# Performance work log

Hardware: AMD Instinct MI355X
Metric: run time of the kernel (lower is better)

Reference implementation:

```python
import jax, jax.numpy as jnp
import numpy as np

IN_FEATURE = 256
OUT_FEATURE = 128
ALPHA = 0.5  # LeakyReLU negative slope
NEG_BIG = -9e15


def setup_inputs() -> dict:
    key = jax.random.key(0)
    k1, k2, k3, k4 = jax.random.split(key, 4)
    N = 8192
    x = jax.random.normal(k1, (N, IN_FEATURE), dtype=jnp.float32)
    adj = jax.random.randint(k2, (N, N), 0, 2, dtype=jnp.int32)
    stdv = 1.0 / np.sqrt(OUT_FEATURE)
    W = jax.random.uniform(k3, (IN_FEATURE, OUT_FEATURE), dtype=jnp.float32,
                           minval=-stdv, maxval=stdv)
    a = jax.random.uniform(k4, (2 * OUT_FEATURE, 1), dtype=jnp.float32,
                           minval=-stdv, maxval=stdv)
    return {"input": x, "adj": adj, "W": W, "a": a}


def reference(input, adj, W, a):
    # h: [N, F_out]
    h = input @ W
    # Additive attention: cat([h_i, h_j]) @ a == h_i @ a1 + h_j @ a2
    a1 = a[:OUT_FEATURE, 0]   # [F_out]
    a2 = a[OUT_FEATURE:, 0]   # [F_out]
    f1 = h @ a1               # [N]  (row / source contribution)
    f2 = h @ a2               # [N]  (col / target contribution)
    e = jax.nn.leaky_relu(f1[:, None] + f2[None, :], negative_slope=ALPHA)  # [N, N]
    scores = jnp.where(adj > 0, e, NEG_BIG)
    attention = jax.nn.softmax(scores, axis=1)  # [N, N]
    h_prime = attention @ h                     # [N, F_out]
    return jax.nn.elu(h_prime)
```

## Files before the change

kernel.cpp:

```cpp
#include <hip/hip_runtime.h>

#define N_NODES 8192
#define IN_F 256
#define OUT_F 128
#define ALPHA 0.5f
#define JC 8
#define KCHUNK 1024
#define RK 128
#define ROUNDS 8
#define RSTEPS 4

using short8 = __attribute__((ext_vector_type(8))) short;
using f32x4  = __attribute__((ext_vector_type(4))) float;

__device__ __forceinline__ unsigned int f2bf(float f){
  unsigned int u = __float_as_uint(f);
  u += 0x7fffu + ((u >> 16) & 1u);
  return u >> 16;
}
__device__ __forceinline__ float bf2f(short s){
  return __uint_as_float(((unsigned int)(unsigned short)s) << 16);
}

__global__ __launch_bounds__(256) void k_h(const float* __restrict__ x,
                                           const float* __restrict__ W,
                                           float* __restrict__ h){
  __shared__ float xs[16*IN_F];
  const int tid = threadIdx.x;
  const int r0 = blockIdx.x * 16;
  const float4* xg = (const float4*)(x + (size_t)r0*IN_F);
  float4* xl = (float4*)xs;
  #pragma unroll
  for(int i=0;i<4;i++) xl[tid + i*256] = xg[tid + i*256];
  __syncthreads();
  const int wave = tid >> 6, lane = tid & 63;
  float2 acc[4];
  #pragma unroll
  for(int j=0;j<4;j++){ acc[j].x = 0.f; acc[j].y = 0.f; }
  const float2* Wp = (const float2*)W;
  for(int k4=0;k4<IN_F;k4+=4){
    float4 xq[4];
    #pragma unroll
    for(int j=0;j<4;j++) xq[j] = *(const float4*)&xs[(wave*4+j)*IN_F + k4];
    #pragma unroll
    for(int kk=0;kk<4;kk++){
      float2 wv = Wp[(size_t)(k4+kk)*64 + lane];
      #pragma unroll
      for(int j=0;j<4;j++){
        float xv = kk==0?xq[j].x : kk==1?xq[j].y : kk==2?xq[j].z : xq[j].w;
        acc[j].x += xv*wv.x; acc[j].y += xv*wv.y;
      }
    }
  }
  #pragma unroll
  for(int j=0;j<4;j++)
    *(float2*)(h + (size_t)(r0 + wave*4 + j)*OUT_F + lane*2) = acc[j];
}

__global__ __launch_bounds__(256) void k_f(const float* __restrict__ h,
                                           const float* __restrict__ a,
                                           float* __restrict__ f1,
                                           float* __restrict__ f2){
  const int wave = threadIdx.x >> 6, lane = threadIdx.x & 63;
  const int row = blockIdx.x*4 + wave;
  float2 hv = ((const float2*)(h + (size_t)row*OUT_F))[lane];
  float2 a1 = ((const float2*)a)[lane];
  float2 a2 = ((const float2*)(a + OUT_F))[lane];
  float s1 = hv.x*a1.x + hv.y*a1.y;
  float s2 = hv.x*a2.x + hv.y*a2.y;
  #pragma unroll
  for(int off=32; off; off>>=1){
    s1 += __shfl_down(s1, off);
    s2 += __shfl_down(s2, off);
  }
  if(lane == 0){ f1[row] = s1; f2[row] = s2; }
}

#define LDW 132
__global__ __launch_bounds__(256) void k_pack(const float* __restrict__ h,
                                              unsigned short* __restrict__ P){
  __shared__ float ld[32*LDW];
  const int tid = threadIdx.x;
  const int kb = blockIdx.x, j0 = kb*32;
  #pragma unroll
  for(int i=0;i<4;i++){
    int idx = tid + i*256;
    int row = idx >> 5, c4 = (idx & 31)*4;
    *(float4*)&ld[row*LDW + c4] = *(const float4*)(h + (size_t)(j0+row)*OUT_F + c4);
  }
  __syncthreads();
  #pragma unroll
  for(int i=0;i<2;i++){
    int o = tid*2 + i;
    int c = o >> 6, lane = o & 63;
    int q = lane >> 4, n = lane & 15;
    short8 v;
    #pragma unroll
    for(int t=0;t<8;t++) v[t] = (short)f2bf(ld[(q*8+t)*LDW + c*16 + n]);
    *(short8*)(P + ((size_t)(kb*8 + c)*64 + lane)*8) = v;
  }
}

__global__ __launch_bounds__(256, 2) void k_attn(const int* __restrict__ adj,
    const unsigned short* __restrict__ P,
    const float* __restrict__ f1, const float* __restrict__ f2,
    float* __restrict__ part, float* __restrict__ denp){
  __shared__ __align__(16) unsigned short Alds[128*RK];
  __shared__ __align__(16) short Blds[RK*OUT_F];
  __shared__ float f1s[128];
  const int tid = threadIdx.x;
  const int wave = tid >> 6, lane = tid & 63;
  const int m = lane & 15, q = lane >> 4;
  const int jc = blockIdx.x;
  const int r0b = blockIdx.y * 128;
  const int jb = jc * KCHUNK;
  const int kb0 = jc * (KCHUNK/32);
  const int srow = tid >> 5;
  const int sc0  = (tid & 31) * 4;
  const int swz  = ((((sc0 >> 3) ^ srow) << 4) | ((sc0 & 4) << 1));

  if(tid < 128) f1s[tid] = f1[r0b + tid];

  f32x4 acc0[8], acc1[8];
  #pragma unroll
  for(int c=0;c<8;c++){ acc0[c] = (f32x4){0,0,0,0}; acc1[c] = (f32x4){0,0,0,0}; }
  float den0 = 0.f, den1 = 0.f;

  const char* Ab = (const char*)Alds;
  char* Aw = (char*)Alds + swz;
  const int mw = m & 7;
  const int rg0 = wave*32 + m;

  __syncthreads();

  for(int rd=0; rd<ROUNDS; rd++){
    const int kbase = jb + rd*RK;
    const int4* Pb = (const int4*)(P + ((size_t)(kb0 + rd*4) << 12));
    int4* Bl4 = (int4*)Blds;
    #pragma unroll
    for(int i=0;i<8;i++) Bl4[i*256 + tid] = Pb[i*256 + tid];
    float4 fv = *(const float4*)(f2 + kbase + sc0);
    const char* ap = (const char*)adj + (((size_t)(r0b + srow)*N_NODES + kbase + sc0) << 2);
    #pragma unroll 4
    for(int i=0;i<16;i++){
      int4 av = *(const int4*)(ap + ((size_t)i*8*N_NODES << 2));
      float f1v = f1s[i*8 + srow];
      float t0 = f1v + fv.x, t1 = f1v + fv.y, t2 = f1v + fv.z, t3 = f1v + fv.w;
      t0 = t0 > 0.f ? t0 : ALPHA*t0;  t1 = t1 > 0.f ? t1 : ALPHA*t1;
      t2 = t2 > 0.f ? t2 : ALPHA*t2;  t3 = t3 > 0.f ? t3 : ALPHA*t3;
      float w0 = av.x > 0 ? __expf(t0) : 0.f;
      float w1 = av.y > 0 ? __expf(t1) : 0.f;
      float w2 = av.z > 0 ? __expf(t2) : 0.f;
      float w3 = av.w > 0 ? __expf(t3) : 0.f;
      uint2 pk;
      pk.x = f2bf(w0) | (f2bf(w1) << 16);
      pk.y = f2bf(w2) | (f2bf(w3) << 16);
      *(uint2*)(Aw + (i*8 + srow)*(RK*2)) = pk;
    }
    __syncthreads();
    #pragma unroll
    for(int s=0;s<RSTEPS;s++){
      const int gq = ((s*4 + q) ^ mw) << 4;
      short8 A0 = *(const short8*)(Ab + rg0*(RK*2) + gq);
      short8 A1 = *(const short8*)(Ab + (rg0+16)*(RK*2) + gq);
      #pragma unroll
      for(int t=0;t<8;t++){ den0 += bf2f(A0[t]); den1 += bf2f(A1[t]); }
      const short8* Bl = (const short8*)Blds + s*512 + lane;
      #pragma unroll
      for(int c=0;c<8;c++){
        short8 Bf = Bl[c*64];
        acc0[c] = __builtin_amdgcn_mfma_f32_16x16x32_bf16(A0, Bf, acc0[c], 0,0,0);
        acc1[c] = __builtin_amdgcn_mfma_f32_16x16x32_bf16(A1, Bf, acc1[c], 0,0,0);
      }
    }
    __syncthreads();
  }

  den0 += __shfl_down(den0, 32); den0 += __shfl_down(den0, 16);
  den1 += __shfl_down(den1, 32); den1 += __shfl_down(den1, 16);
  const int r0w = r0b + wave*32;
  if(lane < 16){
    denp[(size_t)jc*N_NODES + r0w + lane]      = den0;
    denp[(size_t)jc*N_NODES + r0w + 16 + lane] = den1;
  }
  float* pp = part + (size_t)jc*N_NODES*OUT_F;
  #pragma unroll
  for(int c=0;c<8;c++){
    #pragma unroll
    for(int reg=0;reg<4;reg++){
      pp[(size_t)(r0w + q*4 + reg)*OUT_F      + c*16 + m] = acc0[c][reg];
      pp[(size_t)(r0w + 16 + q*4 + reg)*OUT_F + c*16 + m] = acc1[c][reg];
    }
  }
}

__global__ __launch_bounds__(256) void k_out(const float* __restrict__ part,
    const float* __restrict__ denp, float* __restrict__ out){
  const int idx = blockIdx.x*256 + threadIdx.x;
  const int r = idx >> 7;
  float v = 0.f, d = 0.f;
  #pragma unroll
  for(int p=0;p<JC;p++){
    v += part[(size_t)p*N_NODES*OUT_F + idx];
    d += denp[(size_t)p*N_NODES + r];
  }
  v /= d;
  out[idx] = v > 0.f ? v : (__expf(v) - 1.f);
}

extern "C" void kernel_launch(void* const* d_in, const int* in_sizes, int n_in,
                              void* d_out, int out_size, void* d_ws, size_t ws_size,
                              hipStream_t stream){
  const float* x   = (const float*)d_in[0];
  const int*   adj = (const int*)d_in[1];
  const float* W   = (const float*)d_in[2];
  const float* a   = (const float*)d_in[3];
  char* ws = (char*)d_ws;
  float* h            = (float*)ws;
  unsigned short* P   = (unsigned short*)(ws + (4u<<20));
  float* f1           = (float*)(ws + (6u<<20));
  float* f2           = (float*)(ws + (6u<<20) + (32u<<10));
  float* part         = (float*)(ws + (8u<<20));
  float* denp         = (float*)(ws + (40u<<20));
  float* out          = (float*)d_out;

  k_h<<<512, 256, 0, stream>>>(x, W, h);
  k_f<<<2048, 256, 0, stream>>>(h, a, f1, f2);
  k_pack<<<256, 256, 0, stream>>>(h, P);
  k_attn<<<dim3(JC,64), 256, 0, stream>>>(adj, P, f1, f2, part, denp);
  k_out<<<(N_NODES*OUT_F)/256, 256, 0, stream>>>(part, denp, out);
}
```

Before: 410.3 us.

## Double-buffer adj and P via async global-to-LDS loads, compute weights in registers

The attention kernel now uses global_load_lds to stream adjacency tiles and packed h tiles straight into double-buffered shared memory, prefetching the next round while the current one is processed. The round size drops from 128 to 32 columns. Each lane reads its adj values in MFMA fragment order from a swizzled LDS layout and computes the bf16 attention weights in registers, which removes the LDS write and reread of the A tile. The denominator is now summed from fp32 weights instead of rounded bf16 values. In exchange the kernel uses more shared memory and takes more barriers, and it depends on the load-to-LDS completion being waited on before each barrier.

```diff
diff --git a/kernel.cpp b/kernel.cpp
--- a/kernel.cpp
+++ b/kernel.cpp
@@ -6,9 +6,8 @@
 #define ALPHA 0.5f
 #define JC 8
 #define KCHUNK 1024
-#define RK 128
-#define ROUNDS 8
-#define RSTEPS 4
+#define RK 32
+#define ROUNDS 32
 
 using short8 = __attribute__((ext_vector_type(8))) short;
 using f32x4  = __attribute__((ext_vector_type(4))) float;
@@ -18,8 +17,11 @@
   u += 0x7fffu + ((u >> 16) & 1u);
   return u >> 16;
 }
-__device__ __forceinline__ float bf2f(short s){
-  return __uint_as_float(((unsigned int)(unsigned short)s) << 16);
+
+__device__ __forceinline__ void gld16(const void* g, void* l){
+  __builtin_amdgcn_global_load_lds(
+      (const __attribute__((address_space(1))) unsigned int*)g,
+      (__attribute__((address_space(3))) unsigned int*)l, 16, 0, 0);
 }
 
 __global__ __launch_bounds__(256) void k_h(const float* __restrict__ x,
@@ -105,8 +107,9 @@
     const unsigned short* __restrict__ P,
     const float* __restrict__ f1, const float* __restrict__ f2,
     float* __restrict__ part, float* __restrict__ denp){
-  __shared__ __align__(16) unsigned short Alds[128*RK];
-  __shared__ __align__(16) short Blds[RK*OUT_F];
+  __shared__ __align__(16) char Alds[2][16384];
+  __shared__ __align__(16) char Blds[2][8192];
+  __shared__ float f2s[KCHUNK];
   __shared__ float f1s[128];
   const int tid = threadIdx.x;
   const int wave = tid >> 6, lane = tid & 63;
@@ -114,64 +117,76 @@
   const int jc = blockIdx.x;
   const int r0b = blockIdx.y * 128;
   const int jb = jc * KCHUNK;
-  const int kb0 = jc * (KCHUNK/32);
-  const int srow = tid >> 5;
-  const int sc0  = (tid & 31) * 4;
-  const int swz  = ((((sc0 >> 3) ^ srow) << 4) | ((sc0 & 4) << 1));
-
+
+  ((float4*)f2s)[tid] = ((const float4*)(f2 + jb))[tid];
   if(tid < 128) f1s[tid] = f1[r0b + tid];
+
+  const int g = (lane & 7) ^ (lane >> 3);
+  const char* asrc[4];
+  #pragma unroll
+  for(int i=0;i<4;i++){
+    int rowid = (wave*4 + i)*8 + (lane >> 3);
+    asrc[i] = (const char*)(adj + (size_t)(r0b + rowid)*N_NODES + jb) + g*16;
+  }
+  const char* bsrc[2];
+  #pragma unroll
+  for(int i=0;i<2;i++)
+    bsrc[i] = (const char*)P + (size_t)jc*ROUNDS*8192 + ((size_t)(wave*2+i)*64 + lane)*16;
+
+  auto issue_dma = [&](int rd, int buf){
+    #pragma unroll
+    for(int i=0;i<4;i++)
+      gld16(asrc[i] + (size_t)rd*128, Alds[buf] + (wave*4+i)*1024 + lane*16);
+    #pragma unroll
+    for(int i=0;i<2;i++)
+      gld16(bsrc[i] + (size_t)rd*8192, Blds[buf] + (wave*2+i)*1024 + lane*16);
+  };
+
+  issue_dma(0, 0);
 
   f32x4 acc0[8], acc1[8];
   #pragma unroll
   for(int c=0;c<8;c++){ acc0[c] = (f32x4){0,0,0,0}; acc1[c] = (f32x4){0,0,0,0}; }
   float den0 = 0.f, den1 = 0.f;
 
-  const char* Ab = (const char*)Alds;
-  char* Aw = (char*)Alds + swz;
-  const int mw = m & 7;
   const int rg0 = wave*32 + m;
+  const int xr = m & 7;
+  const int s0 = (q*2) ^ xr, s1 = s0 ^ 1;
 
   __syncthreads();
+  const float rf1a = f1s[rg0];
+  const float rf1b = f1s[rg0 + 16];
+
+  auto wcalc = [&](int4 alo, int4 ahi, float4 fva, float4 fvb,
+                   float rf1, float& den) -> short8 {
+    short8 af; float t, w;
+    #define WE(slot, av, fv)                              \
+      t = rf1 + (fv); t = fmaxf(t, ALPHA*t);              \
+      w = ((av) > 0) ? __expf(t) : 0.f;                   \
+      den += w; af[slot] = (short)f2bf(w);
+    WE(0,alo.x,fva.x) WE(1,alo.y,fva.y) WE(2,alo.z,fva.z) WE(3,alo.w,fva.w)
+    WE(4,ahi.x,fvb.x) WE(5,ahi.y,fvb.y) WE(6,ahi.z,fvb.z) WE(7,ahi.w,fvb.w)
+    #undef WE
+    return af;
+  };
 
   for(int rd=0; rd<ROUNDS; rd++){
-    const int kbase = jb + rd*RK;
-    const int4* Pb = (const int4*)(P + ((size_t)(kb0 + rd*4) << 12));
-    int4* Bl4 = (int4*)Blds;
-    #pragma unroll
-    for(int i=0;i<8;i++) Bl4[i*256 + tid] = Pb[i*256 + tid];
-    float4 fv = *(const float4*)(f2 + kbase + sc0);
-    const char* ap = (const char*)adj + (((size_t)(r0b + srow)*N_NODES + kbase + sc0) << 2);
-    #pragma unroll 4
-    for(int i=0;i<16;i++){
-      int4 av = *(const int4*)(ap + ((size_t)i*8*N_NODES << 2));
-      float f1v = f1s[i*8 + srow];
-      float t0 = f1v + fv.x, t1 = f1v + fv.y, t2 = f1v + fv.z, t3 = f1v + fv.w;
-      t0 = t0 > 0.f ? t0 : ALPHA*t0;  t1 = t1 > 0.f ? t1 : ALPHA*t1;
-      t2 = t2 > 0.f ? t2 : ALPHA*t2;  t3 = t3 > 0.f ? t3 : ALPHA*t3;
-      float w0 = av.x > 0 ? __expf(t0) : 0.f;
-      float w1 = av.y > 0 ? __expf(t1) : 0.f;
-      float w2 = av.z > 0 ? __expf(t2) : 0.f;
-      float w3 = av.w > 0 ? __expf(t3) : 0.f;
-      uint2 pk;
-      pk.x = f2bf(w0) | (f2bf(w1) << 16);
-      pk.y = f2bf(w2) | (f2bf(w3) << 16);
-      *(uint2*)(Aw + (i*8 + srow)*(RK*2)) = pk;
-    }
-    __syncthreads();
-    #pragma unroll
-    for(int s=0;s<RSTEPS;s++){
-      const int gq = ((s*4 + q) ^ mw) << 4;
-      short8 A0 = *(const short8*)(Ab + rg0*(RK*2) + gq);
-      short8 A1 = *(const short8*)(Ab + (rg0+16)*(RK*2) + gq);
-      #pragma unroll
-      for(int t=0;t<8;t++){ den0 += bf2f(A0[t]); den1 += bf2f(A1[t]); }
-      const short8* Bl = (const short8*)Blds + s*512 + lane;
-      #pragma unroll
-      for(int c=0;c<8;c++){
-        short8 Bf = Bl[c*64];
-        acc0[c] = __builtin_amdgcn_mfma_f32_16x16x32_bf16(A0, Bf, acc0[c], 0,0,0);
-        acc1[c] = __builtin_amdgcn_mfma_f32_16x16x32_bf16(A1, Bf, acc1[c], 0,0,0);
-      }
+    const int buf = rd & 1;
+    if(rd+1 < ROUNDS) issue_dma(rd+1, buf ^ 1);
+    const int4* Arow0 = (const int4*)(Alds[buf] + rg0*128);
+    const int4* Arow1 = (const int4*)(Alds[buf] + (rg0+16)*128);
+    int4 alo0 = Arow0[s0], ahi0 = Arow0[s1];
+    int4 alo1 = Arow1[s0], ahi1 = Arow1[s1];
+    float4 fva = *(const float4*)(f2s + rd*RK + q*8);
+    float4 fvb = *(const float4*)(f2s + rd*RK + q*8 + 4);
+    short8 af0 = wcalc(alo0, ahi0, fva, fvb, rf1a, den0);
+    short8 af1 = wcalc(alo1, ahi1, fva, fvb, rf1b, den1);
+    const short8* Bl = (const short8*)(Blds[buf]) + lane;
+    #pragma unroll
+    for(int c=0;c<8;c++){
+      short8 Bf = Bl[c*64];
+      acc0[c] = __builtin_amdgcn_mfma_f32_16x16x32_bf16(af0, Bf, acc0[c], 0,0,0);
+      acc1[c] = __builtin_amdgcn_mfma_f32_16x16x32_bf16(af1, Bf, acc1[c], 0,0,0);
     }
     __syncthreads();
   }
```

After: 446.5 us. 1.09x slower.
